# Performance work log

Hardware: AMD Instinct MI355X
Metric: run time of the kernel (lower is better)

Reference implementation:

```python
import jax, jax.numpy as jnp
import numpy as np

H = 1024          # hidden_size
E = 2             # expand factor
D = H * E         # d_inner = 2048
N = 16            # state_size
K = 4             # conv kernel
R = H // 16       # dt_rank = 64
B_SZ = 2
L = 1024
EPS = 1e-6


def setup_inputs() -> dict:
    key = jax.random.key(0)
    ks = jax.random.split(key, 12)
    s = 0.02
    inputs = jax.random.normal(ks[0], (B_SZ, L, H), jnp.float32)
    current_state = jnp.zeros((B_SZ, D, N), jnp.float32)
    norm_w = jnp.ones((H,), jnp.float32)
    in_proj_w = jax.random.normal(ks[1], (2 * D, H), jnp.float32) * s
    in_proj_b = jnp.zeros((2 * D,), jnp.float32)
    conv_w = jax.random.normal(ks[2], (D, 1, K), jnp.float32) * 0.2
    conv_b = jnp.zeros((D,), jnp.float32)
    x_proj_w = jax.random.normal(ks[3], (R + 2 * N, D), jnp.float32) * s
    x_proj_b = jnp.zeros((R + 2 * N,), jnp.float32)
    dt_proj_w = jax.random.normal(ks[4], (D, R), jnp.float32) * s
    dt_proj_b = jnp.zeros((D,), jnp.float32)
    A_log = jnp.log(jnp.tile(jnp.arange(1, N + 1, dtype=jnp.float32)[None, :], (D, 1)))
    D_param = jnp.ones((D,), jnp.float32)
    out_proj_w = jax.random.normal(ks[5], (H, D), jnp.float32) * s
    out_proj_b = jnp.zeros((H,), jnp.float32)
    return dict(inputs=inputs, current_state=current_state, norm_w=norm_w,
                in_proj_w=in_proj_w, in_proj_b=in_proj_b, conv_w=conv_w, conv_b=conv_b,
                x_proj_w=x_proj_w, x_proj_b=x_proj_b, dt_proj_w=dt_proj_w, dt_proj_b=dt_proj_b,
                A_log=A_log, D_param=D_param, out_proj_w=out_proj_w, out_proj_b=out_proj_b)


def _rmsnorm(x, w, eps=EPS):
    var = jnp.mean(x * x, axis=-1, keepdims=True)
    return x * jax.lax.rsqrt(var + eps) * w


def _ssm_forward(inputs, current_state, norm_w, in_proj_w, in_proj_b, conv_w, conv_b,
                 x_proj_w, x_proj_b, dt_proj_w, dt_proj_b, A_log, D_param,
                 out_proj_w, out_proj_b):
    residual = inputs  # standard residual: connect_width -> (inputs, None)
    x = _rmsnorm(inputs, norm_w)                                   # [B,L,H]
    xg = jnp.einsum('blh,oh->blo', x, in_proj_w) + in_proj_b       # [B,L,2D]
    x, gate = jnp.split(xg, 2, axis=-1)                            # each [B,L,D]
    # depthwise causal conv: torch pads K-1 both sides then slices [:L] == left-pad K-1
    xc = jax.lax.conv_general_dilated(
        x.transpose(0, 2, 1), conv_w, window_strides=(1,),
        padding=[(K - 1, 0)], dimension_numbers=('NCH', 'OIH', 'NCH'),
        feature_group_count=D) + conv_b[None, :, None]
    x = jax.nn.silu(xc.transpose(0, 2, 1))                         # [B,L,D]
    proj = jnp.einsum('bld,od->blo', x, x_proj_w) + x_proj_b       # [B,L,R+2N]
    dt, Bm, Cm = proj[..., :R], proj[..., R:R + N], proj[..., R + N:]
    delta = jax.nn.softplus(jnp.einsum('blr,dr->bld', dt, dt_proj_w) + dt_proj_b)  # [B,L,D]
    A = -jnp.exp(A_log)                                            # [D,N]
    log_deltaA = delta[..., None] * A                              # [B,L,D,N] (== log(exp(.)))
    cumsum_deltaA = jnp.exp(jnp.cumsum(log_deltaA, axis=1))        # [B,L,D,N]
    h0_contribution = current_state[:, None] * cumsum_deltaA
    shifted = jnp.concatenate(
        [jnp.ones_like(cumsum_deltaA[:, :1]), cumsum_deltaA[:, :-1]], axis=1)
    deltaB_x = delta[..., None] * Bm[:, :, None, :] * x[..., None] # [B,L,D,N]
    scaled = deltaB_x / jnp.clip(shifted, 1e-10)
    h = jnp.cumsum(scaled, axis=1) * shifted + h0_contribution     # [B,L,D,N]
    y = jnp.sum(h * Cm[:, :, None, :], axis=-1) + x * D_param      # [B,L,D]
    y = y * jax.nn.silu(gate)
    out = jnp.einsum('bld,hd->blh', y, out_proj_w) + out_proj_b    # [B,L,H]
    return residual + out


def reference(inputs, current_state, norm_w, in_proj_w, in_proj_b, conv_w, conv_b,
              x_proj_w, x_proj_b, dt_proj_w, dt_proj_b, A_log, D_param,
              out_proj_w, out_proj_b):
    return _ssm_forward(inputs, current_state, norm_w, in_proj_w, in_proj_b,
                        conv_w, conv_b, x_proj_w, x_proj_b, dt_proj_w, dt_proj_b,
                        A_log, D_param, out_proj_w, out_proj_b)
```

## Files before the change

kernel.cpp:

```cpp
#include <hip/hip_runtime.h>
#include <stdint.h>

#define LSEQ 1024
#define HDIM 1024
#define DDIM 2048
#define BL 2048
#define NST 16
#define XR 1027

typedef unsigned short u16;
typedef __attribute__((ext_vector_type(8))) short bf16x8;
typedef __attribute__((ext_vector_type(4))) float f32x4;

static __device__ __forceinline__ float silu_f(float v) {
  return v * __builtin_amdgcn_rcpf(1.f + __expf(-v));
}
static __device__ __forceinline__ float bf2f(u16 u) {
  union { float f; unsigned int i; } c; c.i = ((unsigned int)u) << 16; return c.f;
}
static __device__ __forceinline__ u16 f2bf(float f) {
  union { float f; unsigned int i; } c; c.f = f;
  unsigned int r = c.i + 0x7fffu + ((c.i >> 16) & 1u);
  return (u16)(r >> 16);
}
static __device__ __forceinline__ float softplus_f(float v) {
  return (v > 20.f) ? v : __logf(1.f + __expf(v));
}

__global__ __launch_bounds__(256) void k_prep(const float* __restrict__ w1,
                                              u16* __restrict__ w1b,
                                              const float* __restrict__ wo,
                                              u16* __restrict__ wob,
                                              const float* __restrict__ xpw,
                                              u16* __restrict__ whb,
                                              u16* __restrict__ wlb,
                                              u16* __restrict__ xgb) {
  int bidx = blockIdx.x;
  int t = threadIdx.x;
  if (bidx < 4096) {
    int idx = bidx * 256 + t;
    float4 v = ((const float4*)w1)[idx];
    ushort4 o;
    o.x = f2bf(v.x); o.y = f2bf(v.y); o.z = f2bf(v.z); o.w = f2bf(v.w);
    ((ushort4*)w1b)[idx] = o;
  } else if (bidx < 6144) {
    int idx = (bidx - 4096) * 256 + t;
    float4 v = ((const float4*)wo)[idx];
    ushort4 o;
    o.x = f2bf(v.x); o.y = f2bf(v.y); o.z = f2bf(v.z); o.w = f2bf(v.w);
    ((ushort4*)wob)[idx] = o;
  } else if (bidx < 6336) {
    int idx = (bidx - 6144) * 256 + t;
    float4 v = ((const float4*)xpw)[idx];
    ushort4 h, l;
    h.x = f2bf(v.x); l.x = f2bf(v.x - bf2f(h.x));
    h.y = f2bf(v.y); l.y = f2bf(v.y - bf2f(h.y));
    h.z = f2bf(v.z); l.z = f2bf(v.z - bf2f(h.z));
    h.w = f2bf(v.w); l.w = f2bf(v.w - bf2f(h.w));
    ((ushort4*)whb)[idx] = h;
    ((ushort4*)wlb)[idx] = l;
  } else {
    int idx = (bidx - 6336) * 256 + t;
    int b = idx / 3072;
    int r = idx - b * 3072;
    ushort4 z4 = {0, 0, 0, 0};
    ((ushort4*)(xgb + (size_t)b * XR * 4096))[r] = z4;
  }
}

__global__ __launch_bounds__(256) void k_rowscale2(const float* __restrict__ inp,
                                                   const float* __restrict__ nw,
                                                   u16* __restrict__ xnb) {
  int row = blockIdx.x;
  int t = threadIdx.x;
  float4 xv = *(const float4*)(inp + (size_t)row * HDIM + t * 4);
  float ss = xv.x * xv.x + xv.y * xv.y + xv.z * xv.z + xv.w * xv.w;
  for (int off = 32; off > 0; off >>= 1) ss += __shfl_down(ss, off);
  __shared__ float red[4];
  if ((t & 63) == 0) red[t >> 6] = ss;
  __syncthreads();
  float tot = red[0] + red[1] + red[2] + red[3];
  float scale = rsqrtf(tot * (1.f / HDIM) + 1e-6f);
  float4 nv = *(const float4*)(nw + t * 4);
  ushort4 o;
  o.x = f2bf(xv.x * scale * nv.x); o.y = f2bf(xv.y * scale * nv.y);
  o.z = f2bf(xv.z * scale * nv.z); o.w = f2bf(xv.w * scale * nv.w);
  ((ushort4*)xnb)[row * 256 + t] = o;
}

__global__ __launch_bounds__(256) void k_gemm1b(const u16* __restrict__ A,
                                                const u16* __restrict__ W,
                                                const float* __restrict__ bias,
                                                u16* __restrict__ xgb) {
  __shared__ u16 Asm[128 * 40];
  __shared__ u16 Wsm[128 * 40];
  int t = threadIdx.x;
  int m0 = blockIdx.y * 128, n0 = blockIdx.x * 128;
  int srow = t >> 1, koff = (t & 1) * 16;
  const u16* Ag = A + (size_t)(m0 + srow) * HDIM + koff;
  const u16* Wg = W + (size_t)(n0 + srow) * HDIM + koff;
  int w = t >> 6, lane = t & 63;
  int wr = w >> 1, wc = w & 1;
  int quad = lane >> 4, mr = lane & 15;
  f32x4 z = {0.f, 0.f, 0.f, 0.f};
  f32x4 acc[4][4] = {{z, z, z, z}, {z, z, z, z}, {z, z, z, z}, {z, z, z, z}};
  const u16* arp = &Asm[(wr * 64 + mr) * 40 + quad * 8];
  const u16* brp = &Wsm[(wc * 64 + mr) * 40 + quad * 8];
  for (int k0 = 0; k0 < HDIM; k0 += 32) {
    uint4 a0 = *(const uint4*)(Ag + k0);
    uint4 a1 = *(const uint4*)(Ag + k0 + 8);
    uint4 w0 = *(const uint4*)(Wg + k0);
    uint4 w1 = *(const uint4*)(Wg + k0 + 8);
    __syncthreads();
    *(uint4*)(&Asm[srow * 40 + koff]) = a0;
    *(uint4*)(&Asm[srow * 40 + koff + 8]) = a1;
    *(uint4*)(&Wsm[srow * 40 + koff]) = w0;
    *(uint4*)(&Wsm[srow * 40 + koff + 8]) = w1;
    __syncthreads();
    bf16x8 af[4], bf[4];
#pragma unroll
    for (int i = 0; i < 4; i++) {
      af[i] = *(const bf16x8*)(arp + i * 16 * 40);
      bf[i] = *(const bf16x8*)(brp + i * 16 * 40);
    }
#pragma unroll
    for (int mi = 0; mi < 4; mi++)
#pragma unroll
      for (int ni = 0; ni < 4; ni++)
        acc[mi][ni] = __builtin_amdgcn_mfma_f32_16x16x32_bf16(af[mi], bf[ni],
                                                              acc[mi][ni], 0, 0, 0);
  }
#pragma unroll
  for (int ni = 0; ni < 4; ni++) {
    int col = n0 + wc * 64 + ni * 16 + mr;
    float bv = bias[col];
#pragma unroll
    for (int mi = 0; mi < 4; mi++) {
#pragma unroll
      for (int rr2 = 0; rr2 < 4; rr2++) {
        int rr = m0 + wr * 64 + mi * 16 + quad * 4 + rr2;
        int row = (rr >> 10) * XR + 3 + (rr & 1023);
        xgb[(size_t)row * 4096 + col] = f2bf(acc[mi][ni][rr2] + bv);
      }
    }
  }
}

__global__ __launch_bounds__(256) void k_xT(const u16* __restrict__ xgb,
                                            u16* __restrict__ xT) {
  __shared__ u16 tile[64][66];
  int dt = blockIdx.x & 31;
  int tt = blockIdx.x >> 5;
  int gtok0 = tt << 6;
  int b = gtok0 >> 10, l0 = gtok0 & 1023;
  int d0 = dt << 6;
  int t = threadIdx.x;
  const u16* src = xgb + (size_t)(b * XR + 3 + l0) * 4096 + d0;
#pragma unroll
  for (int i = 0; i < 8; i++) {
    int idx = t + i * 256;
    int row = idx >> 5, uc = idx & 31;
    unsigned int v = *(const unsigned int*)(src + (size_t)row * 4096 + uc * 2);
    tile[row][uc * 2]     = (u16)(v & 0xffffu);
    tile[row][uc * 2 + 1] = (u16)(v >> 16);
  }
  __syncthreads();
#pragma unroll
  for (int i = 0; i < 8; i++) {
    int idx = t + i * 256;
    int r = idx >> 5, c2 = idx & 31;
    unsigned int lo = tile[c2 * 2][r];
    unsigned int hi = tile[c2 * 2 + 1][r];
    *(unsigned int*)(xT + (size_t)(d0 + r) * 2048 + gtok0 + c2 * 2) = lo | (hi << 16);
  }
}

__global__ __launch_bounds__(256) void k_gemm2b(const u16* __restrict__ A,
                                                const u16* __restrict__ W,
                                                float* __restrict__ psplit) {
  __shared__ u16 Asm[128 * 40];
  __shared__ u16 Wsm[64 * 40];
  int t = threadIdx.x;
  int m0 = blockIdx.y * 128, n0 = blockIdx.x * 64;
  int kstart = blockIdx.z << 10;
  float* outp = psplit + (size_t)blockIdx.z * 2048 * 1024;
  int srow = t >> 1, koff = (t & 1) * 16;
  const u16* Ag = A + (size_t)(m0 + srow) * DDIM + kstart + koff;
  const u16* Wg = W + (size_t)(n0 + (srow & 63)) * DDIM + kstart + koff;
  int w = t >> 6, lane = t & 63;
  int wr = w >> 1, wc = w & 1;
  int quad = lane >> 4, mr = lane & 15;
  f32x4 z = {0.f, 0.f, 0.f, 0.f};
  f32x4 acc[4][2] = {{z, z}, {z, z}, {z, z}, {z, z}};
  const u16* arp = &Asm[(wr * 64 + mr) * 40 + quad * 8];
  const u16* brp = &Wsm[(wc * 32 + mr) * 40 + quad * 8];
  for (int k0 = 0; k0 < 1024; k0 += 32) {
    uint4 a0 = *(const uint4*)(Ag + k0);
    uint4 a1 = *(const uint4*)(Ag + k0 + 8);
    uint4 w0, w1;
    if (t < 128) {
      w0 = *(const uint4*)(Wg + k0);
      w1 = *(const uint4*)(Wg + k0 + 8);
    }
    __syncthreads();
    *(uint4*)(&Asm[srow * 40 + koff]) = a0;
    *(uint4*)(&Asm[srow * 40 + koff + 8]) = a1;
    if (t < 128) {
      *(uint4*)(&Wsm[srow * 40 + koff]) = w0;
      *(uint4*)(&Wsm[srow * 40 + koff + 8]) = w1;
    }
    __syncthreads();
    bf16x8 af[4], bf[2];
#pragma unroll
    for (int i = 0; i < 4; i++) af[i] = *(const bf16x8*)(arp + i * 16 * 40);
#pragma unroll
    for (int i = 0; i < 2; i++) bf[i] = *(const bf16x8*)(brp + i * 16 * 40);
#pragma unroll
    for (int mi = 0; mi < 4; mi++)
#pragma unroll
      for (int ni = 0; ni < 2; ni++)
        acc[mi][ni] = __builtin_amdgcn_mfma_f32_16x16x32_bf16(af[mi], bf[ni],
                                                              acc[mi][ni], 0, 0, 0);
  }
#pragma unroll
  for (int ni = 0; ni < 2; ni++) {
    int col = n0 + wc * 32 + ni * 16 + mr;
#pragma unroll
    for (int mi = 0; mi < 4; mi++) {
#pragma unroll
      for (int rr2 = 0; rr2 < 4; rr2++) {
        int row = m0 + wr * 64 + mi * 16 + quad * 4 + rr2;
        outp[(size_t)row * 1024 + col] = acc[mi][ni][rr2];
      }
    }
  }
}

__global__ __launch_bounds__(256) void k_ocomb(const float* __restrict__ psplit,
                                               const float* __restrict__ bias,
                                               const float* __restrict__ resid,
                                               float* __restrict__ out) {
  int idx = blockIdx.x * 256 + threadIdx.x;
  int colf = idx & 255;
  float4 a = ((const float4*)psplit)[idx];
  float4 b2 = ((const float4*)(psplit + 2048 * 1024))[idx];
  float4 rv = ((const float4*)resid)[idx];
  float4 bv = *(const float4*)(bias + colf * 4);
  float4 o;
  o.x = a.x + b2.x + bv.x + rv.x;
  o.y = a.y + b2.y + bv.y + rv.y;
  o.z = a.z + b2.z + bv.z + rv.z;
  o.w = a.w + b2.w + bv.w + rv.w;
  ((float4*)out)[idx] = o;
}

__global__ __launch_bounds__(256) void k_xprojT(const u16* __restrict__ xgb,
                                                const u16* __restrict__ whb,
                                                const u16* __restrict__ wlb,
                                                const float* __restrict__ cw,
                                                const float* __restrict__ cb,
                                                float* __restrict__ projT,
                                                float* __restrict__ pscr) {
  __shared__ u16 Xst[67 * 40];
  __shared__ u16 XH[64 * 40];
  __shared__ u16 XL[64 * 40];
  __shared__ u16 WH[96 * 40];
  __shared__ u16 WL[96 * 40];
  int t = threadIdx.x;
  int tt = blockIdx.x & 31, ks = blockIdx.x >> 5;
  int tokbase = tt << 6;
  int b = tokbase >> 10, l0 = tokbase & 1023;
  int kbase = ks << 7;
  const u16* xbase = xgb + (size_t)(b * XR + l0) * 4096;
  float* outp = (ks == 0) ? projT : (pscr + (size_t)(ks - 1) * 196608);
  int dlane = t & 31, tokg = t >> 5;
  int wvq = t >> 6, lane = t & 63;
  int quad = lane >> 4, mr = lane & 15;
  f32x4 z = {0.f, 0.f, 0.f, 0.f};
  f32x4 acc[6] = {z, z, z, z, z, z};

  for (int it = 0; it < 4; it++) {
    int kc = kbase + (it << 5);
    for (int idx = t; idx < 268; idx += 256) {
      int r = idx >> 2, p = idx & 3;
      uint4 v = *(const uint4*)(xbase + (size_t)r * 4096 + kc + p * 8);
      *(uint4*)(&Xst[r * 40 + p * 8]) = v;
    }
    for (int idx = t; idx < 384; idx += 256) {
      int r = idx >> 2, p = idx & 3;
      *(uint4*)(&WH[r * 40 + p * 8]) = *(const uint4*)(whb + (size_t)r * 2048 + kc + p * 8);
      *(uint4*)(&WL[r * 40 + p * 8]) = *(const uint4*)(wlb + (size_t)r * 2048 + kc + p * 8);
    }
    __syncthreads();
    {
      int d = kc + dlane;
      float4 cwv = *(const float4*)(cw + d * 4);
      float cbv = cb[d];
      float xr[11];
#pragma unroll
      for (int j = 0; j < 11; j++) xr[j] = bf2f(Xst[(tokg * 8 + j) * 40 + dlane]);
#pragma unroll
      for (int jj = 0; jj < 8; jj++) {
        float xc = silu_f(cbv + cwv.x * xr[jj] + cwv.y * xr[jj + 1] +
                          cwv.z * xr[jj + 2] + cwv.w * xr[jj + 3]);
        u16 h = f2bf(xc);
        u16 l = f2bf(xc - bf2f(h));
        XH[(tokg * 8 + jj) * 40 + dlane] = h;
        XL[(tokg * 8 + jj) * 40 + dlane] = l;
      }
    }
    __syncthreads();
    bf16x8 xh = *(const bf16x8*)(&XH[(wvq * 16 + mr) * 40 + quad * 8]);
    bf16x8 xl = *(const bf16x8*)(&XL[(wvq * 16 + mr) * 40 + quad * 8]);
#pragma unroll
    for (int mi = 0; mi < 6; mi++) {
      bf16x8 wh = *(const bf16x8*)(&WH[(mi * 16 + mr) * 40 + quad * 8]);
      bf16x8 wl = *(const bf16x8*)(&WL[(mi * 16 + mr) * 40 + quad * 8]);
      acc[mi] = __builtin_amdgcn_mfma_f32_16x16x32_bf16(wh, xh, acc[mi], 0, 0, 0);
      acc[mi] = __builtin_amdgcn_mfma_f32_16x16x32_bf16(wh, xl, acc[mi], 0, 0, 0);
      acc[mi] = __builtin_amdgcn_mfma_f32_16x16x32_bf16(wl, xh, acc[mi], 0, 0, 0);
    }
    __syncthreads();
  }
#pragma unroll
  for (int mi = 0; mi < 6; mi++) {
#pragma unroll
    for (int rr = 0; rr < 4; rr++) {
      int o = mi * 16 + quad * 4 + rr;
      outp[(size_t)o * BL + tokbase + wvq * 16 + mr] = acc[mi][rr];
    }
  }
}

__global__ __launch_bounds__(256) void k_xcomb(float* __restrict__ projT,
                                               const float* __restrict__ scr,
                                               const float* __restrict__ xpb) {
  int idx = blockIdx.x * 256 + threadIdx.x;
  int o = idx >> 9;
  float4 a = ((const float4*)projT)[idx];
  float bv = xpb[o];
  float sx = bv, sy = bv, sz = bv, sw = bv;
#pragma unroll
  for (int p = 0; p < 15; p++) {
    float4 s = ((const float4*)(scr + (size_t)p * 196608))[idx];
    sx += s.x; sy += s.y; sz += s.z; sw += s.w;
  }
  a.x += sx; a.y += sy; a.z += sz; a.w += sw;
  ((float4*)projT)[idx] = a;
}

__global__ __launch_bounds__(256) void k_delta(const float* __restrict__ projT,
                                               const float* __restrict__ dtw,
                                               const float* __restrict__ dtb,
                                               float* __restrict__ deltaT) {
  __shared__ float dw_s[16][64];
  int t = threadIdx.x;
  int d0 = (blockIdx.x >> 3) * 16;
  int tokbase = (blockIdx.x & 7) * 256;
  {
    const float* src = dtw + (size_t)d0 * 64;
#pragma unroll
    for (int i = 0; i < 4; i++) {
      int idx = t + i * 256;
      dw_s[idx >> 6][idx & 63] = src[idx];
    }
  }
  __syncthreads();
  int tq = t & 63, dq = t >> 6;
  const float* pr = projT + tokbase + tq * 4;
  int dbase = d0 + dq * 4;
  float acc[4][4];
#pragma unroll
  for (int di = 0; di < 4; di++) {
    float bv = dtb[dbase + di];
    acc[di][0] = bv; acc[di][1] = bv; acc[di][2] = bv; acc[di][3] = bv;
  }
#pragma unroll 8
  for (int r = 0; r < 64; r++) {
    float4 pv = *(const float4*)(pr + (size_t)r * BL);
#pragma unroll
    for (int di = 0; di < 4; di++) {
      float wk = dw_s[dq * 4 + di][r];
      acc[di][0] += pv.x * wk; acc[di][1] += pv.y * wk;
      acc[di][2] += pv.z * wk; acc[di][3] += pv.w * wk;
    }
  }
#pragma unroll
  for (int di = 0; di < 4; di++) {
    float4 o;
    o.x = softplus_f(acc[di][0]); o.y = softplus_f(acc[di][1]);
    o.z = softplus_f(acc[di][2]); o.w = softplus_f(acc[di][3]);
    *(float4*)(deltaT + (size_t)(dbase + di) * BL + tokbase + tq * 4) = o;
  }
}

__global__ __launch_bounds__(256) void k_scan2(const float* __restrict__ projT,
                                               const float* __restrict__ deltaT,
                                               const u16* __restrict__ xT,
                                               const u16* __restrict__ xgb,
                                               const float* __restrict__ cw,
                                               const float* __restrict__ cb,
                                               const float* __restrict__ alog,
                                               const float* __restrict__ dparam,
                                               const float* __restrict__ cs,
                                               u16* __restrict__ yb) {
  __shared__ float wtot[4];
  __shared__ float xcp[1088];
  __shared__ float uvl[1088];
  __shared__ float dlp[1088];

  int t = threadIdx.x;
  int cidx = ((blockIdx.x & 7) << 9) | (blockIdx.x >> 3);
  int b = cidx >> 11;
  int d = cidx & (DDIM - 1);
  int wv = t >> 6, lane = t & 63;

  float4 cwv = *(const float4*)(cw + d * 4);
  float cbv = cb[d];
  float Dp = dparam[d];
  const u16* gcol = xgb + (size_t)(b * XR + 3) * 4096 + d + DDIM;
  u16* ycol = yb + ((size_t)(b << 10)) * DDIM + d;
  int colbase = b << 10;
  int tok0 = t << 2;

  float4 dv = *(const float4*)(deltaT + (size_t)d * BL + colbase + tok0);

  float* xls = dlp;
  if (t < 3) xls[t] = 0.f;
  {
    ushort4 xv = ((const ushort4*)(xT + (size_t)d * 2048 + colbase))[t];
    xls[3 + tok0 + 0] = bf2f(xv.x);
    xls[3 + tok0 + 1] = bf2f(xv.y);
    xls[3 + tok0 + 2] = bf2f(xv.z);
    xls[3 + tok0 + 3] = bf2f(xv.w);
  }
  __syncthreads();

#pragma unroll
  for (int i = 0; i < 4; i++) {
    int tok = tok0 + i;
    float xc = silu_f(cbv + cwv.x * xls[tok] + cwv.y * xls[tok + 1] +
                      cwv.z * xls[tok + 2] + cwv.w * xls[tok + 3]);
    xcp[((tok >> 4) * 17) + (tok & 15)] = xc;
  }
  float d0 = dv.x, d1 = dv.y, d2 = dv.z, d3 = dv.w;
  uvl[((tok0 >> 4) * 17) + (tok0 & 15)]             = d0;
  uvl[(((tok0 + 1) >> 4) * 17) + ((tok0 + 1) & 15)] = d1;
  uvl[(((tok0 + 2) >> 4) * 17) + ((tok0 + 2) & 15)] = d2;
  uvl[(((tok0 + 3) >> 4) * 17) + ((tok0 + 3) & 15)] = d3;
  float c0 = d0, c1 = c0 + d1, c2 = c1 + d2, c3 = c2 + d3;
  float sc = c3;
#pragma unroll
  for (int off = 1; off < 64; off <<= 1) {
    float u = __shfl_up(sc, off);
    if (lane >= off) sc += u;
  }
  if (lane == 63) wtot[wv] = sc;
  __syncthreads();
  {
    float base = sc - c3;
#pragma unroll
    for (int i = 0; i < 3; i++) if (i < wv) base += wtot[i];
    dlp[((tok0 >> 4) * 17) + (tok0 & 15)]             = base + c0;
    dlp[(((tok0 + 1) >> 4) * 17) + ((tok0 + 1) & 15)] = base + c1;
    dlp[(((tok0 + 2) >> 4) * 17) + ((tok0 + 2) & 15)] = base + c2;
    dlp[(((tok0 + 3) >> 4) * 17) + ((tok0 + 3) & 15)] = base + c3;
  }
#pragma unroll
  for (int i = 0; i < 4; i++) {
    int tok = tok0 + i;
    int p = ((tok >> 4) * 17) + (tok & 15);
    uvl[p] = uvl[p] * xcp[p];
  }
  __syncthreads();

  int pb = lane * 17;
  float y[16];
#pragma unroll
  for (int i = 0; i < 16; i++) y[i] = 0.f;
  float Dprev = (lane == 0) ? 0.f : dlp[pb - 2];

#pragma unroll 1
  for (int r = 0; r < 4; r++) {
    int n = (wv << 2) + r;
    float An = -__expf(alog[d * NST + n]);
    float st = cs[(size_t)(b * DDIM + d) * NST + n];
    const float* pB = projT + (size_t)(64 + n) * BL + colbase + (lane << 4);
    const float* pC = pB + (size_t)16 * BL;
    float Pp = __expf(An * Dprev);
    float sl = 0.f;
#pragma unroll
    for (int c = 0; c < 4; c++) {
      float4 bv = *(const float4*)(pB + c * 4);
      float4 cv = *(const float4*)(pC + c * 4);
      float bvs[4] = {bv.x, bv.y, bv.z, bv.w};
      float cvs[4] = {cv.x, cv.y, cv.z, cv.w};
#pragma unroll
      for (int j = 0; j < 4; j++) {
        int i = c * 4 + j;
        float P = __expf(An * dlp[pb + i]);
        float w = uvl[pb + i] * bvs[j] * __builtin_amdgcn_rcpf(fmaxf(Pp, 1e-10f));
        sl += w;
        y[i] += (sl * Pp + st * P) * cvs[j];
        Pp = P;
      }
    }
    float s2 = sl;
#pragma unroll
    for (int off = 1; off < 64; off <<= 1) {
      float u = __shfl_up(s2, off);
      if (lane >= off) s2 += u;
    }
    float Soff = s2 - sl;
#pragma unroll
    for (int c = 0; c < 4; c++) {
      float4 cv = *(const float4*)(pC + c * 4);
      float cvs[4] = {cv.x, cv.y, cv.z, cv.w};
#pragma unroll
      for (int j = 0; j < 4; j++) {
        int i = c * 4 + j;
        float dlm = (i == 0) ? Dprev : dlp[pb + i - 1];
        y[i] += Soff * __expf(An * dlm) * cvs[j];
      }
    }
  }
  __syncthreads();
  if (wv == 2) {
#pragma unroll
    for (int i = 0; i < 16; i++) uvl[pb + i] = y[i];
  } else if (wv == 3) {
#pragma unroll
    for (int i = 0; i < 16; i++) dlp[pb + i] = y[i];
  }
  __syncthreads();
  if (wv == 0) {
#pragma unroll
    for (int i = 0; i < 16; i++) uvl[pb + i] += y[i];
  } else if (wv == 1) {
#pragma unroll
    for (int i = 0; i < 16; i++) dlp[pb + i] += y[i];
  }
  __syncthreads();
#pragma unroll
  for (int i = 0; i < 4; i++) {
    int tok = tok0 + i;
    int p = ((tok >> 4) * 17) + (tok & 15);
    float yv = uvl[p] + dlp[p] + xcp[p] * Dp;
    float g = bf2f(gcol[(size_t)tok * 4096]);
    ycol[(size_t)tok * DDIM] = f2bf(yv * silu_f(g));
  }
}

extern "C" void kernel_launch(void* const* d_in, const int* in_sizes, int n_in,
                              void* d_out, int out_size, void* d_ws, size_t ws_size,
                              hipStream_t stream) {
  const float* inp    = (const float*)d_in[0];
  const float* cstate = (const float*)d_in[1];
  const float* norm_w = (const float*)d_in[2];
  const float* w1     = (const float*)d_in[3];
  const float* b1     = (const float*)d_in[4];
  const float* convw  = (const float*)d_in[5];
  const float* convb  = (const float*)d_in[6];
  const float* xpw    = (const float*)d_in[7];
  const float* xpb    = (const float*)d_in[8];
  const float* dtw    = (const float*)d_in[9];
  const float* dtb    = (const float*)d_in[10];
  const float* alog   = (const float*)d_in[11];
  const float* dparam = (const float*)d_in[12];
  const float* wo     = (const float*)d_in[13];
  const float* bo     = (const float*)d_in[14];
  float* out = (float*)d_out;

  char* wsb = (char*)d_ws;
  u16*   w1b    = (u16*)(wsb + 0);
  u16*   xTbuf  = w1b;
  u16*   wob    = (u16*)(wsb + 8388608);
  u16*   whb    = (u16*)(wsb + 12591104);
  u16*   wlb    = (u16*)(wsb + 12984320);
  float* projT  = (float*)(wsb + 13377536);
  u16*   xgb    = (u16*)(wsb + 14163968);
  u16*   yb     = (u16*)(wsb + 30990336);
  u16*   xnb    = yb;
  float* deltaT = (float*)(wsb + 39378944);
  float* pscr   = deltaT;
  float* psplit = deltaT;

  k_prep<<<6360, 256, 0, stream>>>(w1, w1b, wo, wob, xpw, whb, wlb, xgb);
  k_rowscale2<<<BL, 256, 0, stream>>>(inp, norm_w, xnb);
  k_gemm1b<<<dim3(32, 16), 256, 0, stream>>>(xnb, w1b, b1, xgb);
  k_xT<<<1024, 256, 0, stream>>>(xgb, xTbuf);
  k_xprojT<<<512, 256, 0, stream>>>(xgb, whb, wlb, convw, convb, projT, pscr);
  k_xcomb<<<192, 256, 0, stream>>>(projT, pscr, xpb);
  k_delta<<<1024, 256, 0, stream>>>(projT, dtw, dtb, deltaT);
  k_scan2<<<2 * DDIM, 256, 0, stream>>>(projT, deltaT, xTbuf, xgb, convw, convb,
                                        alog, dparam, cstate, yb);
  k_gemm2b<<<dim3(16, 16, 2), 256, 0, stream>>>(yb, wob, psplit);
  k_ocomb<<<2048, 256, 0, stream>>>(psplit, bo, inp, out);
}
```

Measured before the change: 274.2 us.

## Move scan gating into a transposing kernel and fold rmsnorm into prep

The scan kernel now writes its pre-gate output as contiguous float4 rows into the delta buffer, in place. A new tiled transpose kernel then applies the SiLU gate and writes the bf16 token-major output with coalesced accesses. This replaces the strided per-token gate loads and stores that the scan kernel used to do. Separately, the RMSNorm row-scaling kernel is merged into the prep kernel as extra blocks, which removes one launch. In exchange there is one more kernel and an extra float round trip of the scan output through global memory.

```diff
diff --git a/kernel.cpp b/kernel.cpp
--- a/kernel.cpp
+++ b/kernel.cpp
@@ -34,7 +34,10 @@
                                               const float* __restrict__ xpw,
                                               u16* __restrict__ whb,
                                               u16* __restrict__ wlb,
-                                              u16* __restrict__ xgb) {
+                                              u16* __restrict__ xgb,
+                                              const float* __restrict__ inp,
+                                              const float* __restrict__ nw,
+                                              u16* __restrict__ xnb) {
   int bidx = blockIdx.x;
   int t = threadIdx.x;
   if (bidx < 4096) {
@@ -59,33 +62,28 @@
     h.w = f2bf(v.w); l.w = f2bf(v.w - bf2f(h.w));
     ((ushort4*)whb)[idx] = h;
     ((ushort4*)wlb)[idx] = l;
-  } else {
+  } else if (bidx < 6360) {
     int idx = (bidx - 6336) * 256 + t;
     int b = idx / 3072;
     int r = idx - b * 3072;
     ushort4 z4 = {0, 0, 0, 0};
     ((ushort4*)(xgb + (size_t)b * XR * 4096))[r] = z4;
-  }
-}
-
-__global__ __launch_bounds__(256) void k_rowscale2(const float* __restrict__ inp,
-                                                   const float* __restrict__ nw,
-                                                   u16* __restrict__ xnb) {
-  int row = blockIdx.x;
-  int t = threadIdx.x;
-  float4 xv = *(const float4*)(inp + (size_t)row * HDIM + t * 4);
-  float ss = xv.x * xv.x + xv.y * xv.y + xv.z * xv.z + xv.w * xv.w;
-  for (int off = 32; off > 0; off >>= 1) ss += __shfl_down(ss, off);
-  __shared__ float red[4];
-  if ((t & 63) == 0) red[t >> 6] = ss;
-  __syncthreads();
-  float tot = red[0] + red[1] + red[2] + red[3];
-  float scale = rsqrtf(tot * (1.f / HDIM) + 1e-6f);
-  float4 nv = *(const float4*)(nw + t * 4);
-  ushort4 o;
-  o.x = f2bf(xv.x * scale * nv.x); o.y = f2bf(xv.y * scale * nv.y);
-  o.z = f2bf(xv.z * scale * nv.z); o.w = f2bf(xv.w * scale * nv.w);
-  ((ushort4*)xnb)[row * 256 + t] = o;
+  } else {
+    int row = bidx - 6360;
+    float4 xv = *(const float4*)(inp + (size_t)row * HDIM + t * 4);
+    float ss = xv.x * xv.x + xv.y * xv.y + xv.z * xv.z + xv.w * xv.w;
+    for (int off = 32; off > 0; off >>= 1) ss += __shfl_down(ss, off);
+    __shared__ float red[4];
+    if ((t & 63) == 0) red[t >> 6] = ss;
+    __syncthreads();
+    float tot = red[0] + red[1] + red[2] + red[3];
+    float scale = rsqrtf(tot * (1.f / HDIM) + 1e-6f);
+    float4 nv = *(const float4*)(nw + t * 4);
+    ushort4 o;
+    o.x = f2bf(xv.x * scale * nv.x); o.y = f2bf(xv.y * scale * nv.y);
+    o.z = f2bf(xv.z * scale * nv.z); o.w = f2bf(xv.w * scale * nv.w);
+    ((ushort4*)xnb)[row * 256 + t] = o;
+  }
 }
 
 __global__ __launch_bounds__(256) void k_gemm1b(const u16* __restrict__ A,
@@ -395,15 +393,13 @@
 }
 
 __global__ __launch_bounds__(256) void k_scan2(const float* __restrict__ projT,
-                                               const float* __restrict__ deltaT,
+                                               float* __restrict__ deltaT,
                                                const u16* __restrict__ xT,
-                                               const u16* __restrict__ xgb,
                                                const float* __restrict__ cw,
                                                const float* __restrict__ cb,
                                                const float* __restrict__ alog,
                                                const float* __restrict__ dparam,
-                                               const float* __restrict__ cs,
-                                               u16* __restrict__ yb) {
+                                               const float* __restrict__ cs) {
   __shared__ float wtot[4];
   __shared__ float xcp[1088];
   __shared__ float uvl[1088];
@@ -418,12 +414,11 @@
   float4 cwv = *(const float4*)(cw + d * 4);
   float cbv = cb[d];
   float Dp = dparam[d];
-  const u16* gcol = xgb + (size_t)(b * XR + 3) * 4096 + d + DDIM;
-  u16* ycol = yb + ((size_t)(b << 10)) * DDIM + d;
   int colbase = b << 10;
   int tok0 = t << 2;
-
-  float4 dv = *(const float4*)(deltaT + (size_t)d * BL + colbase + tok0);
+  float* drow = deltaT + (size_t)d * BL + colbase;
+
+  float4 dv = *(const float4*)(drow + tok0);
 
   float* xls = dlp;
   if (t < 3) xls[t] = 0.f;
@@ -541,13 +536,44 @@
     for (int i = 0; i < 16; i++) dlp[pb + i] += y[i];
   }
   __syncthreads();
-#pragma unroll
-  for (int i = 0; i < 4; i++) {
-    int tok = tok0 + i;
-    int p = ((tok >> 4) * 17) + (tok & 15);
-    float yv = uvl[p] + dlp[p] + xcp[p] * Dp;
-    float g = bf2f(gcol[(size_t)tok * 4096]);
-    ycol[(size_t)tok * DDIM] = f2bf(yv * silu_f(g));
+  {
+    float4 yo;
+    int p0 = ((tok0 >> 4) * 17) + (tok0 & 15);
+    int p1 = (((tok0 + 1) >> 4) * 17) + ((tok0 + 1) & 15);
+    int p2 = (((tok0 + 2) >> 4) * 17) + ((tok0 + 2) & 15);
+    int p3 = (((tok0 + 3) >> 4) * 17) + ((tok0 + 3) & 15);
+    yo.x = uvl[p0] + dlp[p0] + xcp[p0] * Dp;
+    yo.y = uvl[p1] + dlp[p1] + xcp[p1] * Dp;
+    yo.z = uvl[p2] + dlp[p2] + xcp[p2] * Dp;
+    yo.w = uvl[p3] + dlp[p3] + xcp[p3] * Dp;
+    *(float4*)(drow + tok0) = yo;
+  }
+}
+
+__global__ __launch_bounds__(256) void k_gate(const float* __restrict__ yT,
+                                              const u16* __restrict__ xgb,
+                                              u16* __restrict__ yb) {
+  __shared__ float tile[64 * 65];
+  int dt = blockIdx.x & 31;
+  int tt = blockIdx.x >> 5;
+  int gtok0 = tt << 6;
+  int b = gtok0 >> 10, l0 = gtok0 & 1023;
+  int d0 = dt << 6;
+  int t = threadIdx.x;
+#pragma unroll
+  for (int i = 0; i < 16; i++) {
+    int idx = t + i * 256;
+    int r = idx >> 6, c = idx & 63;
+    tile[r * 65 + c] = yT[(size_t)(d0 + r) * BL + gtok0 + c];
+  }
+  __syncthreads();
+#pragma unroll
+  for (int i = 0; i < 16; i++) {
+    int idx = t + i * 256;
+    int tr = idx >> 6, dc = idx & 63;
+    float g = bf2f(xgb[(size_t)(b * XR + 3 + l0 + tr) * 4096 + 2048 + d0 + dc]);
+    float yv = tile[dc * 65 + tr];
+    yb[(size_t)(gtok0 + tr) * DDIM + d0 + dc] = f2bf(yv * silu_f(g));
   }
 }
 
@@ -585,15 +611,16 @@
   float* pscr   = deltaT;
   float* psplit = deltaT;
 
-  k_prep<<<6360, 256, 0, stream>>>(w1, w1b, wo, wob, xpw, whb, wlb, xgb);
-  k_rowscale2<<<BL, 256, 0, stream>>>(inp, norm_w, xnb);
+  k_prep<<<8408, 256, 0, stream>>>(w1, w1b, wo, wob, xpw, whb, wlb, xgb,
+                                   inp, norm_w, xnb);
   k_gemm1b<<<dim3(32, 16), 256, 0, stream>>>(xnb, w1b, b1, xgb);
   k_xT<<<1024, 256, 0, stream>>>(xgb, xTbuf);
   k_xprojT<<<512, 256, 0, stream>>>(xgb, whb, wlb, convw, convb, projT, pscr);
   k_xcomb<<<192, 256, 0, stream>>>(projT, pscr, xpb);
   k_delta<<<1024, 256, 0, stream>>>(projT, dtw, dtb, deltaT);
-  k_scan2<<<2 * DDIM, 256, 0, stream>>>(projT, deltaT, xTbuf, xgb, convw, convb,
-                                        alog, dparam, cstate, yb);
+  k_scan2<<<2 * DDIM, 256, 0, stream>>>(projT, deltaT, xTbuf, convw, convb,
+                                        alog, dparam, cstate);
+  k_gate<<<1024, 256, 0, stream>>>(deltaT, xgb, yb);
   k_gemm2b<<<dim3(16, 16, 2), 256, 0, stream>>>(yb, wob, psplit);
   k_ocomb<<<2048, 256, 0, stream>>>(psplit, bo, inp, out);
 }
```

Measured after the change: 261.8 us. 4.5% less time.
